# Performance work log

Hardware: AMD Instinct MI355X
Metric: run time of the kernel (lower is better)

## Reference

```python
import jax, jax.numpy as jnp
import numpy as np

SCALE = 0.02

def setup_inputs() -> dict:
    key = jax.random.key(0)
    k1, k2 = jax.random.split(key)
    B, D, T, H = 2, 1024, 2048, 16
    x = jax.random.normal(k1, (B, D, T), dtype=jnp.float32)
    qkv = jax.random.normal(k2, (3, H, D, D // H), dtype=jnp.float32) * SCALE
    return {"x": x, "qkv": qkv}

def reference(x, qkv):
    B, D, T = x.shape
    H = qkv.shape[1]
    # fused QKV projection: (B,D,T) x (3,H,D,Dh) -> (3,B,H,T,Dh)
    proj = jnp.einsum('bdt,nhdD->nbhtD', x, qkv)
    q, k, v = proj[0], proj[1], proj[2]
    scale = jnp.sqrt(jnp.asarray(D // H, dtype=x.dtype))
    # scores: (B,H,T,T)
    attn = jax.nn.softmax(jnp.einsum('bhtD,bhTD->bhtT', q, k) / scale, axis=-1)
    # weighted values, head dim placed before time: (B,H,Dh,T)
    out = jnp.einsum('bhtT,bhTD->bhDt', attn, v)
    return out.reshape(B, D, T)
```

## Files before the change

kernel.cpp:

```cpp
#include <hip/hip_runtime.h>

#define B_ 2
#define D_ 1024
#define T_ 2048
#define H_ 16
#define DH_ 64
#define BH_ (B_ * H_)

typedef __attribute__((ext_vector_type(8))) short bf16x8;
typedef __attribute__((ext_vector_type(8))) unsigned short u16x8;
typedef __attribute__((ext_vector_type(4))) float f32x4;

__device__ __forceinline__ unsigned short f2bf(float f) {
    unsigned u = __float_as_uint(f);
    u += 0x7fffu + ((u >> 16) & 1u);
    return (unsigned short)(u >> 16);
}

__global__ __launch_bounds__(256) void xpose_kernel(
    const float* __restrict__ x, unsigned short* __restrict__ xT)
{
    __shared__ __align__(16) unsigned short Ls[64][68];
    const int t0 = blockIdx.x * 64;
    const int d0 = blockIdx.y * 64;
    const int b  = blockIdx.z;
    const int tid = threadIdx.x;

    const float* xb = x + (size_t)b * D_ * T_ + (size_t)d0 * T_ + t0;
    #pragma unroll
    for (int p = 0; p < 4; p++) {
        int i4  = tid + p * 256;
        int row = i4 >> 4;
        int c4  = (i4 & 15) << 2;
        float4 v = *(const float4*)(xb + (size_t)row * T_ + c4);
        ushort4 u;
        u.x = f2bf(v.x); u.y = f2bf(v.y); u.z = f2bf(v.z); u.w = f2bf(v.w);
        *(ushort4*)&Ls[row][c4] = u;
    }
    __syncthreads();
    unsigned short* ob = xT + (size_t)b * T_ * D_ + (size_t)t0 * D_ + d0;
    #pragma unroll
    for (int p = 0; p < 2; p++) {
        int i    = tid + p * 256;
        int orow = i >> 3;
        int oc8  = (i & 7) * 8;
        u16x8 tv;
        #pragma unroll
        for (int j = 0; j < 8; j++) tv[j] = Ls[oc8 + j][orow];
        *(u16x8*)(ob + (size_t)orow * D_ + oc8) = tv;
    }
}

__global__ __launch_bounds__(256) void wpose_kernel(
    const float* __restrict__ w, unsigned short* __restrict__ wT)
{
    __shared__ __align__(16) unsigned short Ls[64][68];
    const int d0 = blockIdx.x * 64;
    const int nh = blockIdx.y;
    const int tid = threadIdx.x;

    const float* wb = w + (size_t)nh * D_ * DH_ + (size_t)d0 * DH_;
    #pragma unroll
    for (int p = 0; p < 4; p++) {
        int i4  = tid + p * 256;
        int row = i4 >> 4;
        int c4  = (i4 & 15) << 2;
        float4 v = *(const float4*)(wb + (size_t)row * DH_ + c4);
        ushort4 u;
        u.x = f2bf(v.x); u.y = f2bf(v.y); u.z = f2bf(v.z); u.w = f2bf(v.w);
        *(ushort4*)&Ls[row][c4] = u;
    }
    __syncthreads();
    unsigned short* ob = wT + (size_t)nh * DH_ * D_ + d0;
    #pragma unroll
    for (int p = 0; p < 2; p++) {
        int i    = tid + p * 256;
        int orow = i >> 3;
        int oc8  = (i & 7) * 8;
        u16x8 tv;
        #pragma unroll
        for (int j = 0; j < 8; j++) tv[j] = Ls[oc8 + j][orow];
        *(u16x8*)(ob + (size_t)orow * D_ + oc8) = tv;
    }
}

#define LX 72

__global__ __launch_bounds__(256) void proj_mfma_kernel(
    const unsigned short* __restrict__ xT, const unsigned short* __restrict__ wT,
    unsigned short* __restrict__ qkv)
{
    __shared__ __align__(16) unsigned short Buf[18432];
    unsigned short* Xs = Buf;
    unsigned short* Ws = Buf + 9216;
    unsigned short* Es = Buf;

    const int t0 = blockIdx.x * 128;
    const int y  = blockIdx.y;
    const int n  = y >> 4;
    const int b  = (y >> 3) & 1;
    const int hp = y & 7;

    const unsigned short* xb = xT + (size_t)b * T_ * D_ + (size_t)t0 * D_;
    const unsigned short* wb = wT + (size_t)(n * 16 + 2 * hp) * DH_ * D_;

    const int tid  = threadIdx.x;
    const int wv   = tid >> 6;
    const int lane = tid & 63;
    const int c15  = lane & 15;
    const int quad = lane >> 4;
    const int tq   = (wv & 1) * 64;
    const int dq   = (wv >> 1) * 64;

    f32x4 acc[4][4];
    #pragma unroll
    for (int mt = 0; mt < 4; mt++)
        #pragma unroll
        for (int nt = 0; nt < 4; nt++)
            acc[mt][nt] = (f32x4){0.f, 0.f, 0.f, 0.f};

    for (int k0 = 0; k0 < D_; k0 += 64) {
        __syncthreads();
        #pragma unroll
        for (int p = 0; p < 4; p++) {
            int i    = tid + p * 256;
            int row  = i >> 3;
            int col8 = (i & 7) * 8;
            *(u16x8*)&Xs[row * LX + col8] =
                *(const u16x8*)(xb + (size_t)row * D_ + k0 + col8);
            *(u16x8*)&Ws[row * LX + col8] =
                *(const u16x8*)(wb + (size_t)row * D_ + k0 + col8);
        }
        __syncthreads();

        bf16x8 af[4][2], bf[4][2];
        #pragma unroll
        for (int mt = 0; mt < 4; mt++)
            #pragma unroll
            for (int s = 0; s < 2; s++)
                af[mt][s] = *(bf16x8*)&Xs[(tq + mt * 16 + c15) * LX + quad * 8 + s * 32];
        #pragma unroll
        for (int nt = 0; nt < 4; nt++)
            #pragma unroll
            for (int s = 0; s < 2; s++)
                bf[nt][s] = *(bf16x8*)&Ws[(dq + nt * 16 + c15) * LX + quad * 8 + s * 32];

        #pragma unroll
        for (int mt = 0; mt < 4; mt++)
            #pragma unroll
            for (int nt = 0; nt < 4; nt++)
                #pragma unroll
                for (int s = 0; s < 2; s++)
                    acc[mt][nt] = __builtin_amdgcn_mfma_f32_16x16x32_bf16(
                        af[mt][s], bf[nt][s], acc[mt][nt], 0, 0, 0);
    }

    const float scale = (n == 0) ? 0.125f : 1.0f;
    __syncthreads();
    #pragma unroll
    for (int mt = 0; mt < 4; mt++)
        #pragma unroll
        for (int nt = 0; nt < 4; nt++)
            #pragma unroll
            for (int r = 0; r < 4; r++)
                Es[(tq + mt * 16 + quad * 4 + r) * 136 + dq + nt * 16 + c15] =
                    f2bf(acc[mt][nt][r] * scale);
    __syncthreads();

    #pragma unroll
    for (int p = 0; p < 8; p++) {
        int i    = tid + p * 256;
        int row  = i >> 4;
        int col8 = (i & 15) * 8;
        int head = col8 >> 6;
        unsigned short* ob = qkv +
            ((size_t)(n * 32 + b * 16 + 2 * hp + head) * T_ + t0 + row) * DH_ + (col8 & 63);
        *(u16x8*)ob = *(u16x8*)&Es[row * 136 + col8];
    }
}

__global__ __launch_bounds__(256) void vpose_kernel(
    const unsigned short* __restrict__ qkv, unsigned short* __restrict__ vT)
{
    __shared__ __align__(16) unsigned short Ls[64][68];
    const int t0 = blockIdx.x * 64;
    const int bh = blockIdx.y;
    const int tid = threadIdx.x;

    const unsigned short* vsrc = qkv + ((size_t)(2 * BH_ + bh) * T_ + t0) * DH_;
    #pragma unroll
    for (int p = 0; p < 2; p++) {
        int i    = tid + p * 256;
        int row  = i >> 3;
        int col8 = (i & 7) * 8;
        *(u16x8*)&Ls[row][col8] = *(const u16x8*)(vsrc + (size_t)row * DH_ + col8);
    }
    __syncthreads();
    unsigned short* ob = vT + (size_t)bh * DH_ * T_ + t0;
    #pragma unroll
    for (int p = 0; p < 2; p++) {
        int i    = tid + p * 256;
        int orow = i >> 3;
        int oc8  = (i & 7) * 8;
        u16x8 tv;
        #pragma unroll
        for (int j = 0; j < 8; j++) tv[j] = Ls[oc8 + j][orow];
        *(u16x8*)(ob + (size_t)orow * T_ + oc8) = tv;
    }
}

#define LQ 72

__global__ __launch_bounds__(256) void attn_mfma_kernel(
    const unsigned short* __restrict__ qkv, const unsigned short* __restrict__ vT,
    float* __restrict__ out)
{
    __shared__ __align__(16) unsigned short Sm[13824];
    unsigned short* Ks = Sm;
    unsigned short* Vs = Sm + 4608;
    unsigned short* Ps = Sm + 9216;
    float*          Os = (float*)Sm;

    const int t0 = blockIdx.x * 64;
    const int bh = blockIdx.y;

    const unsigned short* qg = qkv + ((size_t)bh * T_ + t0) * DH_;
    const unsigned short* kg = qkv + ((size_t)(BH_ + bh) * T_) * DH_;
    const unsigned short* vg = vT + (size_t)bh * DH_ * T_;

    const int tid  = threadIdx.x;
    const int wv   = tid >> 6;
    const int lane = tid & 63;
    const int c15  = lane & 15;
    const int quad = lane >> 4;

    bf16x8 aq[2];
    #pragma unroll
    for (int s = 0; s < 2; s++)
        aq[s] = *(const bf16x8*)(qg + (size_t)(16 * wv + c15) * DH_ + quad * 8 + s * 32);

    float lrow[4] = {0.f, 0.f, 0.f, 0.f};
    f32x4 Oacc[4];
    #pragma unroll
    for (int i = 0; i < 4; i++) Oacc[i] = (f32x4){0.f, 0.f, 0.f, 0.f};

    for (int tau = 0; tau < T_; tau += 64) {
        __syncthreads();
        #pragma unroll
        for (int p = 0; p < 2; p++) {
            int i    = tid + p * 256;
            int row  = i >> 3;
            int col8 = (i & 7) * 8;
            *(u16x8*)&Ks[row * LQ + col8] =
                *(const u16x8*)(kg + (size_t)(tau + row) * DH_ + col8);
            *(u16x8*)&Vs[row * LQ + col8] =
                *(const u16x8*)(vg + (size_t)row * T_ + tau + col8);
        }
        __syncthreads();

        f32x4 S[4];
        #pragma unroll
        for (int j4 = 0; j4 < 4; j4++) {
            f32x4 acc = (f32x4){0.f, 0.f, 0.f, 0.f};
            #pragma unroll
            for (int s = 0; s < 2; s++) {
                bf16x8 bk = *(bf16x8*)&Ks[(j4 * 16 + c15) * LQ + quad * 8 + s * 32];
                acc = __builtin_amdgcn_mfma_f32_16x16x32_bf16(aq[s], bk, acc, 0, 0, 0);
            }
            S[j4] = acc;
        }

        #pragma unroll
        for (int i = 0; i < 4; i++) {
            float p0 = __expf(S[0][i]);
            float p1 = __expf(S[1][i]);
            float p2 = __expf(S[2][i]);
            float p3 = __expf(S[3][i]);
            lrow[i] += (p0 + p1) + (p2 + p3);
            int prow = (16 * wv + quad * 4 + i) * LQ + c15;
            Ps[prow +  0] = f2bf(p0);
            Ps[prow + 16] = f2bf(p1);
            Ps[prow + 32] = f2bf(p2);
            Ps[prow + 48] = f2bf(p3);
        }
        __syncthreads();

        #pragma unroll
        for (int s = 0; s < 2; s++) {
            bf16x8 ap = *(bf16x8*)&Ps[(16 * wv + c15) * LQ + quad * 8 + s * 32];
            #pragma unroll
            for (int j4 = 0; j4 < 4; j4++) {
                bf16x8 bv = *(bf16x8*)&Vs[(j4 * 16 + c15) * LQ + quad * 8 + s * 32];
                Oacc[j4] = __builtin_amdgcn_mfma_f32_16x16x32_bf16(ap, bv, Oacc[j4], 0, 0, 0);
            }
        }
    }

    #pragma unroll
    for (int i = 0; i < 4; i++)
        #pragma unroll
        for (int off = 1; off < 16; off <<= 1)
            lrow[i] += __shfl_xor(lrow[i], off);

    __syncthreads();
    #pragma unroll
    for (int i = 0; i < 4; i++) {
        float inv = 1.0f / lrow[i];
        int r = 16 * wv + quad * 4 + i;
        #pragma unroll
        for (int j4 = 0; j4 < 4; j4++)
            Os[(j4 * 16 + c15) * 68 + r] = Oacc[j4][i] * inv;
    }
    __syncthreads();

    const int b = bh >> 4, h = bh & 15;
    float* og = out + (size_t)b * D_ * T_ + (size_t)(h * DH_) * T_ + t0;
    #pragma unroll
    for (int p = 0; p < 4; p++) {
        int c   = tid + p * 256;
        int row = c >> 4;
        int c4  = (c & 15) << 2;
        float4 v = *(float4*)&Os[row * 68 + c4];
        *(float4*)(og + (size_t)row * T_ + c4) = v;
    }
}

extern "C" void kernel_launch(void* const* d_in, const int* in_sizes, int n_in,
                              void* d_out, int out_size, void* d_ws, size_t ws_size,
                              hipStream_t stream)
{
    const float* x = (const float*)d_in[0];
    const float* w = (const float*)d_in[1];
    float* out = (float*)d_out;

    unsigned short* qkv = (unsigned short*)d_ws;
    unsigned short* vT  = (unsigned short*)((char*)d_ws + (24u << 20));
    unsigned short* xT  = (unsigned short*)((char*)d_ws + (32u << 20));
    unsigned short* wT  = (unsigned short*)((char*)d_ws + (40u << 20));

    xpose_kernel<<<dim3(T_ / 64, D_ / 64, B_), 256, 0, stream>>>(x, xT);
    wpose_kernel<<<dim3(D_ / 64, 3 * H_), 256, 0, stream>>>(w, wT);
    proj_mfma_kernel<<<dim3(T_ / 128, 48), 256, 0, stream>>>(xT, wT, qkv);
    vpose_kernel<<<dim3(T_ / 64, BH_), 256, 0, stream>>>(qkv, vT);
    attn_mfma_kernel<<<dim3(T_ / 64, BH_), 256, 0, stream>>>(qkv, vT, out);
}
```

Baseline: 203.0 us.

## Fuse V transpose into projection and enlarge attention query tile

The projection kernel now writes V directly in transposed (head-dim by time) layout through its shared-memory staging, which removes the separate vpose kernel launch and its extra global round trip. The attention kernel processes 128 queries per block, 32 per wave, so each K/V tile staged in shared memory is reused across twice as many queries, halving K/V reload traffic. It also computes S transposed (K as the A operand) so P is written with packed 64-bit stores, and row sums are combined through shared memory. In exchange, register and LDS use per block rise and the grid has half as many blocks, which may lower occupancy.

New measurement: 203.6 us. About the same (+0.3%).

```diff
diff --git a/kernel.cpp b/kernel.cpp
--- a/kernel.cpp
+++ b/kernel.cpp
@@ -88,7 +88,7 @@
 
 __global__ __launch_bounds__(256) void proj_mfma_kernel(
     const unsigned short* __restrict__ xT, const unsigned short* __restrict__ wT,
-    unsigned short* __restrict__ qkv)
+    unsigned short* __restrict__ qk, unsigned short* __restrict__ vT)
 {
     __shared__ __align__(16) unsigned short Buf[18432];
     unsigned short* Xs = Buf;
@@ -167,65 +167,53 @@
                     f2bf(acc[mt][nt][r] * scale);
     __syncthreads();
 
-    #pragma unroll
-    for (int p = 0; p < 8; p++) {
-        int i    = tid + p * 256;
-        int row  = i >> 4;
-        int col8 = (i & 15) * 8;
-        int head = col8 >> 6;
-        unsigned short* ob = qkv +
-            ((size_t)(n * 32 + b * 16 + 2 * hp + head) * T_ + t0 + row) * DH_ + (col8 & 63);
-        *(u16x8*)ob = *(u16x8*)&Es[row * 136 + col8];
-    }
-}
-
-__global__ __launch_bounds__(256) void vpose_kernel(
-    const unsigned short* __restrict__ qkv, unsigned short* __restrict__ vT)
-{
-    __shared__ __align__(16) unsigned short Ls[64][68];
-    const int t0 = blockIdx.x * 64;
+    if (n < 2) {
+        #pragma unroll
+        for (int p = 0; p < 8; p++) {
+            int i    = tid + p * 256;
+            int row  = i >> 4;
+            int col8 = (i & 15) * 8;
+            int head = col8 >> 6;
+            unsigned short* ob = qk +
+                ((size_t)(n * 32 + b * 16 + 2 * hp + head) * T_ + t0 + row) * DH_ + (col8 & 63);
+            *(u16x8*)ob = *(u16x8*)&Es[row * 136 + col8];
+        }
+    } else {
+        #pragma unroll
+        for (int p = 0; p < 8; p++) {
+            int i    = tid + p * 256;
+            int orow = i >> 4;
+            int oc8  = (i & 15) * 8;
+            int head = orow >> 6;
+            u16x8 tv;
+            #pragma unroll
+            for (int j = 0; j < 8; j++) tv[j] = Es[(oc8 + j) * 136 + orow];
+            unsigned short* ob = vT +
+                (size_t)(b * 16 + 2 * hp + head) * DH_ * T_ +
+                (size_t)(orow & 63) * T_ + t0 + oc8;
+            *(u16x8*)ob = tv;
+        }
+    }
+}
+
+#define LQ 72
+
+__global__ __launch_bounds__(256) void attn_mfma_kernel(
+    const unsigned short* __restrict__ qk, const unsigned short* __restrict__ vT,
+    float* __restrict__ out)
+{
+    __shared__ __align__(16) unsigned char smem[37376];
+    unsigned short* Ks  = (unsigned short*)smem;
+    unsigned short* Vs  = (unsigned short*)(smem + 9216);
+    unsigned short* Psb = (unsigned short*)(smem + 18432);
+    float*          Os  = (float*)smem;
+    float*          Lrow = (float*)(smem + 36864);
+
+    const int t0 = blockIdx.x * 128;
     const int bh = blockIdx.y;
-    const int tid = threadIdx.x;
-
-    const unsigned short* vsrc = qkv + ((size_t)(2 * BH_ + bh) * T_ + t0) * DH_;
-    #pragma unroll
-    for (int p = 0; p < 2; p++) {
-        int i    = tid + p * 256;
-        int row  = i >> 3;
-        int col8 = (i & 7) * 8;
-        *(u16x8*)&Ls[row][col8] = *(const u16x8*)(vsrc + (size_t)row * DH_ + col8);
-    }
-    __syncthreads();
-    unsigned short* ob = vT + (size_t)bh * DH_ * T_ + t0;
-    #pragma unroll
-    for (int p = 0; p < 2; p++) {
-        int i    = tid + p * 256;
-        int orow = i >> 3;
-        int oc8  = (i & 7) * 8;
-        u16x8 tv;
-        #pragma unroll
-        for (int j = 0; j < 8; j++) tv[j] = Ls[oc8 + j][orow];
-        *(u16x8*)(ob + (size_t)orow * T_ + oc8) = tv;
-    }
-}
-
-#define LQ 72
-
-__global__ __launch_bounds__(256) void attn_mfma_kernel(
-    const unsigned short* __restrict__ qkv, const unsigned short* __restrict__ vT,
-    float* __restrict__ out)
-{
-    __shared__ __align__(16) unsigned short Sm[13824];
-    unsigned short* Ks = Sm;
-    unsigned short* Vs = Sm + 4608;
-    unsigned short* Ps = Sm + 9216;
-    float*          Os = (float*)Sm;
-
-    const int t0 = blockIdx.x * 64;
-    const int bh = blockIdx.y;
-
-    const unsigned short* qg = qkv + ((size_t)bh * T_ + t0) * DH_;
-    const unsigned short* kg = qkv + ((size_t)(BH_ + bh) * T_) * DH_;
+
+    const unsigned short* qg = qk + ((size_t)bh * T_ + t0) * DH_;
+    const unsigned short* kg = qk + ((size_t)(BH_ + bh) * T_) * DH_;
     const unsigned short* vg = vT + (size_t)bh * DH_ * T_;
 
     const int tid  = threadIdx.x;
@@ -234,15 +222,23 @@
     const int c15  = lane & 15;
     const int quad = lane >> 4;
 
-    bf16x8 aq[2];
-    #pragma unroll
-    for (int s = 0; s < 2; s++)
-        aq[s] = *(const bf16x8*)(qg + (size_t)(16 * wv + c15) * DH_ + quad * 8 + s * 32);
-
-    float lrow[4] = {0.f, 0.f, 0.f, 0.f};
-    f32x4 Oacc[4];
-    #pragma unroll
-    for (int i = 0; i < 4; i++) Oacc[i] = (f32x4){0.f, 0.f, 0.f, 0.f};
+    unsigned short* Ps = Psb + wv * 2304;
+
+    bf16x8 bq[2][2];
+    #pragma unroll
+    for (int g = 0; g < 2; g++)
+        #pragma unroll
+        for (int s = 0; s < 2; s++)
+            bq[g][s] = *(const bf16x8*)(qg +
+                (size_t)(wv * 32 + g * 16 + c15) * DH_ + quad * 8 + s * 32);
+
+    float lsum[2] = {0.f, 0.f};
+    f32x4 Oacc[2][4];
+    #pragma unroll
+    for (int g = 0; g < 2; g++)
+        #pragma unroll
+        for (int nt = 0; nt < 4; nt++)
+            Oacc[g][nt] = (f32x4){0.f, 0.f, 0.f, 0.f};
 
     for (int tau = 0; tau < T_; tau += 64) {
         __syncthreads();
@@ -258,70 +254,86 @@
         }
         __syncthreads();
 
-        f32x4 S[4];
-        #pragma unroll
-        for (int j4 = 0; j4 < 4; j4++) {
-            f32x4 acc = (f32x4){0.f, 0.f, 0.f, 0.f};
+        bf16x8 ak[4][2];
+        #pragma unroll
+        for (int mt = 0; mt < 4; mt++)
+            #pragma unroll
+            for (int s = 0; s < 2; s++)
+                ak[mt][s] = *(bf16x8*)&Ks[(mt * 16 + c15) * LQ + quad * 8 + s * 32];
+
+        #pragma unroll
+        for (int g = 0; g < 2; g++) {
+            #pragma unroll
+            for (int mt = 0; mt < 4; mt++) {
+                f32x4 sa = (f32x4){0.f, 0.f, 0.f, 0.f};
+                #pragma unroll
+                for (int s = 0; s < 2; s++)
+                    sa = __builtin_amdgcn_mfma_f32_16x16x32_bf16(ak[mt][s], bq[g][s], sa, 0, 0, 0);
+                float p0 = __expf(sa[0]);
+                float p1 = __expf(sa[1]);
+                float p2 = __expf(sa[2]);
+                float p3 = __expf(sa[3]);
+                lsum[g] += (p0 + p1) + (p2 + p3);
+                uint2 pk;
+                pk.x = (unsigned)f2bf(p0) | ((unsigned)f2bf(p1) << 16);
+                pk.y = (unsigned)f2bf(p2) | ((unsigned)f2bf(p3) << 16);
+                *(uint2*)&Ps[(g * 16 + c15) * LQ + mt * 16 + quad * 4] = pk;
+            }
+        }
+        __syncthreads();
+
+        bf16x8 bv[4][2];
+        #pragma unroll
+        for (int nt = 0; nt < 4; nt++)
+            #pragma unroll
+            for (int s = 0; s < 2; s++)
+                bv[nt][s] = *(bf16x8*)&Vs[(nt * 16 + c15) * LQ + quad * 8 + s * 32];
+        #pragma unroll
+        for (int g = 0; g < 2; g++)
             #pragma unroll
             for (int s = 0; s < 2; s++) {
-                bf16x8 bk = *(bf16x8*)&Ks[(j4 * 16 + c15) * LQ + quad * 8 + s * 32];
-                acc = __builtin_amdgcn_mfma_f32_16x16x32_bf16(aq[s], bk, acc, 0, 0, 0);
+                bf16x8 ap = *(bf16x8*)&Ps[(g * 16 + c15) * LQ + quad * 8 + s * 32];
+                #pragma unroll
+                for (int nt = 0; nt < 4; nt++)
+                    Oacc[g][nt] = __builtin_amdgcn_mfma_f32_16x16x32_bf16(
+                        ap, bv[nt][s], Oacc[g][nt], 0, 0, 0);
             }
-            S[j4] = acc;
-        }
-
-        #pragma unroll
-        for (int i = 0; i < 4; i++) {
-            float p0 = __expf(S[0][i]);
-            float p1 = __expf(S[1][i]);
-            float p2 = __expf(S[2][i]);
-            float p3 = __expf(S[3][i]);
-            lrow[i] += (p0 + p1) + (p2 + p3);
-            int prow = (16 * wv + quad * 4 + i) * LQ + c15;
-            Ps[prow +  0] = f2bf(p0);
-            Ps[prow + 16] = f2bf(p1);
-            Ps[prow + 32] = f2bf(p2);
-            Ps[prow + 48] = f2bf(p3);
-        }
-        __syncthreads();
-
-        #pragma unroll
-        for (int s = 0; s < 2; s++) {
-            bf16x8 ap = *(bf16x8*)&Ps[(16 * wv + c15) * LQ + quad * 8 + s * 32];
-            #pragma unroll
-            for (int j4 = 0; j4 < 4; j4++) {
-                bf16x8 bv = *(bf16x8*)&Vs[(j4 * 16 + c15) * LQ + quad * 8 + s * 32];
-                Oacc[j4] = __builtin_amdgcn_mfma_f32_16x16x32_bf16(ap, bv, Oacc[j4], 0, 0, 0);
-            }
-        }
-    }
-
-    #pragma unroll
-    for (int i = 0; i < 4; i++)
-        #pragma unroll
-        for (int off = 1; off < 16; off <<= 1)
-            lrow[i] += __shfl_xor(lrow[i], off);
-
-    __syncthreads();
-    #pragma unroll
-    for (int i = 0; i < 4; i++) {
-        float inv = 1.0f / lrow[i];
-        int r = 16 * wv + quad * 4 + i;
-        #pragma unroll
-        for (int j4 = 0; j4 < 4; j4++)
-            Os[(j4 * 16 + c15) * 68 + r] = Oacc[j4][i] * inv;
+    }
+
+    #pragma unroll
+    for (int g = 0; g < 2; g++) {
+        lsum[g] += __shfl_xor(lsum[g], 16);
+        lsum[g] += __shfl_xor(lsum[g], 32);
+    }
+    if (lane < 16) {
+        Lrow[wv * 32 + lane]      = lsum[0];
+        Lrow[wv * 32 + 16 + lane] = lsum[1];
+    }
+    __syncthreads();
+
+    #pragma unroll
+    for (int g = 0; g < 2; g++) {
+        float linv[4];
+        #pragma unroll
+        for (int r = 0; r < 4; r++)
+            linv[r] = 1.0f / Lrow[wv * 32 + g * 16 + quad * 4 + r];
+        #pragma unroll
+        for (int nt = 0; nt < 4; nt++)
+            #pragma unroll
+            for (int r = 0; r < 4; r++)
+                Os[(nt * 16 + c15) * 132 + wv * 32 + g * 16 + quad * 4 + r] =
+                    Oacc[g][nt][r] * linv[r];
     }
     __syncthreads();
 
     const int b = bh >> 4, h = bh & 15;
     float* og = out + (size_t)b * D_ * T_ + (size_t)(h * DH_) * T_ + t0;
     #pragma unroll
-    for (int p = 0; p < 4; p++) {
-        int c   = tid + p * 256;
-        int row = c >> 4;
-        int c4  = (c & 15) << 2;
-        float4 v = *(float4*)&Os[row * 68 + c4];
-        *(float4*)(og + (size_t)row * T_ + c4) = v;
+    for (int p = 0; p < 8; p++) {
+        int i   = tid + p * 256;
+        int row = i >> 5;
+        int c4  = (i & 31) << 2;
+        *(float4*)(og + (size_t)row * T_ + c4) = *(float4*)&Os[row * 132 + c4];
     }
 }
 
@@ -333,14 +345,13 @@
     const float* w = (const float*)d_in[1];
     float* out = (float*)d_out;
 
-    unsigned short* qkv = (unsigned short*)d_ws;
-    unsigned short* vT  = (unsigned short*)((char*)d_ws + (24u << 20));
-    unsigned short* xT  = (unsigned short*)((char*)d_ws + (32u << 20));
-    unsigned short* wT  = (unsigned short*)((char*)d_ws + (40u << 20));
+    unsigned short* qk = (unsigned short*)d_ws;
+    unsigned short* vT = (unsigned short*)((char*)d_ws + (24u << 20));
+    unsigned short* xT = (unsigned short*)((char*)d_ws + (32u << 20));
+    unsigned short* wT = (unsigned short*)((char*)d_ws + (40u << 20));
 
     xpose_kernel<<<dim3(T_ / 64, D_ / 64, B_), 256, 0, stream>>>(x, xT);
     wpose_kernel<<<dim3(D_ / 64, 3 * H_), 256, 0, stream>>>(w, wT);
-    proj_mfma_kernel<<<dim3(T_ / 128, 48), 256, 0, stream>>>(xT, wT, qkv);
-    vpose_kernel<<<dim3(T_ / 64, BH_), 256, 0, stream>>>(qkv, vT);
-    attn_mfma_kernel<<<dim3(T_ / 64, BH_), 256, 0, stream>>>(qkv, vT, out);
-}
+    proj_mfma_kernel<<<dim3(T_ / 128, 48), 256, 0, stream>>>(xT, wT, qk, vT);
+    attn_mfma_kernel<<<dim3(T_ / 128, BH_), 256, 0, stream>>>(qk, vT, out);
+}
```
